# Optimization experiments

Measured on AMD Instinct MI355X. Metric: run time of the kernel, lower is better.

Reference implementation:

```python
import jax, jax.numpy as jnp
import numpy as np

B, C, IMG = 32, 3, 224
NP = 14            # patches per side
PS = IMG // NP     # 16
IN_DIM = C * PS * PS  # 768
D = 768
NH = 12
DH = D // NH       # 64
L = 12
MLP = 4 * D        # 3072
OUT = 1000
S = NP * NP + 1    # 197
EPS = 1e-5


def _pos_embedding(seq_len, dim):
    i = jnp.arange(seq_len, dtype=jnp.float32)[:, None]
    j = jnp.arange(dim, dtype=jnp.float32)[None, :]
    je = j - jnp.mod(j, 2.0)  # even: j, odd: j-1
    angle = i / jnp.power(10000.0, je / dim)
    return jnp.where(jnp.mod(j, 2.0) == 0, jnp.sin(angle), jnp.cos(angle))


def setup_inputs() -> dict:
    key = jax.random.key(0)
    ks = jax.random.split(key, 24)
    s = 0.02
    inp = {
        "x": jax.random.normal(ks[0], (B, C, IMG, IMG), jnp.float32),
        "cls_emb": jax.random.normal(ks[1], (1, 1, D), jnp.float32),
        "pos": _pos_embedding(S, D),
        "Wmap": jax.random.normal(ks[2], (IN_DIM, D), jnp.float32) * s,
        "bmap": jnp.zeros((D,), jnp.float32),
        "ln1_g": jnp.ones((L, D), jnp.float32),
        "ln1_b": jnp.zeros((L, D), jnp.float32),
        "Wq": jax.random.normal(ks[3], (L, NH, DH, DH), jnp.float32) * s,
        "bq": jnp.zeros((L, NH, DH), jnp.float32),
        "Wk": jax.random.normal(ks[4], (L, NH, DH, DH), jnp.float32) * s,
        "bk": jnp.zeros((L, NH, DH), jnp.float32),
        "Wv": jax.random.normal(ks[5], (L, NH, DH, DH), jnp.float32) * s,
        "bv": jnp.zeros((L, NH, DH), jnp.float32),
        "ln2_g": jnp.ones((L, D), jnp.float32),
        "ln2_b": jnp.zeros((L, D), jnp.float32),
        "W1": jax.random.normal(ks[6], (L, D, MLP), jnp.float32) * s,
        "b1": jnp.zeros((L, MLP), jnp.float32),
        "W2": jax.random.normal(ks[7], (L, MLP, D), jnp.float32) * s,
        "b2": jnp.zeros((L, D), jnp.float32),
        "Wc": jax.random.normal(ks[8], (D, OUT), jnp.float32) * s,
        "bc": jnp.zeros((OUT,), jnp.float32),
    }
    return inp


def _layernorm(x, g, b):
    mu = jnp.mean(x, axis=-1, keepdims=True)
    var = jnp.var(x, axis=-1, keepdims=True)
    return (x - mu) * jax.lax.rsqrt(var + EPS) * g + b


def _patchify(x):
    # [B,C,H,W] -> [B, NP*NP, C*PS*PS], flatten order (c, h, w) per patch
    n = x.shape[0]
    x = x.reshape(n, C, NP, PS, NP, PS)
    x = jnp.transpose(x, (0, 2, 4, 1, 3, 5))  # [B, ph, pw, C, PS, PS]
    return x.reshape(n, NP * NP, IN_DIM)


def reference(x, cls_emb, pos, Wmap, bmap, ln1_g, ln1_b, Wq, bq, Wk, bk, Wv, bv,
              ln2_g, ln2_b, W1, b1, W2, b2, Wc, bc):
    patches = _patchify(x)
    tokens = patches @ Wmap + bmap  # [B, NP*NP, D]
    tokens = jnp.concatenate([jnp.broadcast_to(cls_emb, (x.shape[0], 1, D)), tokens], axis=1)
    out = tokens + pos  # [B, S, D]
    scale = 1.0 / jnp.sqrt(jnp.float32(DH))
    for l in range(L):
        xn = _layernorm(out, ln1_g[l], ln1_b[l])
        xh = xn.reshape(xn.shape[0], S, NH, DH)
        q = jnp.einsum('bshd,hed->bshe', xh, Wq[l]) + bq[l]
        k = jnp.einsum('bshd,hed->bshe', xh, Wk[l]) + bk[l]
        v = jnp.einsum('bshd,hed->bshe', xh, Wv[l]) + bv[l]
        att = jax.nn.softmax(jnp.einsum('bqhd,bkhd->bhqk', q, k) * scale, axis=-1)
        attn_out = jnp.einsum('bhqk,bkhd->bqhd', att, v).reshape(out.shape)
        out = out + attn_out
        xn2 = _layernorm(out, ln2_g[l], ln2_b[l])
        h = jax.nn.gelu(xn2 @ W1[l] + b1[l], approximate=False)
        out = out + (h @ W2[l] + b2[l])
    cls = out[:, 0]
    return jax.nn.softmax(cls @ Wc + bc, axis=-1)
```

## Files before the change

kernel.cpp:

```cpp
#include <hip/hip_runtime.h>
#include <hip/hip_bf16.h>
#include <math.h>

#define VB   32
#define VD   768
#define VNH  12
#define VDH  64
#define VL   12
#define VMLP 3072
#define VOUT 1000
#define VS   197
#define VNPAT 196

typedef _Float16 half8 __attribute__((ext_vector_type(8)));
typedef _Float16 half4 __attribute__((ext_vector_type(4)));
typedef float f32x4 __attribute__((ext_vector_type(4)));

static __device__ __forceinline__ unsigned short f2h(float f) {
  _Float16 h = (_Float16)f;
  return __builtin_bit_cast(unsigned short, h);
}
static __device__ __forceinline__ float h2f(unsigned short u) {
  return (float)__builtin_bit_cast(_Float16, u);
}

static __device__ __forceinline__ void gload_lds16(const void* g, void* l) {
  __builtin_amdgcn_global_load_lds(
      (const __attribute__((address_space(1))) unsigned int*)g,
      (__attribute__((address_space(3))) unsigned int*)l, 16, 0, 0);
}

__global__ __launch_bounds__(256) void patchify_kernel(
    const float* __restrict__ x, unsigned short* __restrict__ P) {
  int bp = blockIdx.x;
  int b = bp / VNPAT, p = bp - b * VNPAT;
  int py = p / 14, px = p - py * 14;
  int t = threadIdx.x;
  int iy = t >> 4, ix = t & 15;
#pragma unroll
  for (int c = 0; c < 3; c++) {
    float val = x[(((size_t)(b * 3 + c) * 224) + (py * 16 + iy)) * 224 + px * 16 + ix];
    P[(size_t)bp * 768 + c * 256 + t] = f2h(val);
  }
}

__global__ __launch_bounds__(256) void transpose_kernel(
    const float* __restrict__ W, unsigned short* __restrict__ WT,
    int K, int N) {
  __shared__ float ts[64][65];
  int n0 = blockIdx.x * 64, k0 = blockIdx.y * 64;
  const float* Wl = W + (size_t)blockIdx.z * K * N;
  unsigned short* WTl = WT + (size_t)blockIdx.z * K * N;
  int t = threadIdx.x;
  int r = t >> 4, c4 = (t & 15) * 4;
#pragma unroll
  for (int p = 0; p < 4; ++p) {
    int row = p * 16 + r;
    float4 v = *(const float4*)(Wl + (size_t)(k0 + row) * N + n0 + c4);
    ts[row][c4 + 0] = v.x; ts[row][c4 + 1] = v.y;
    ts[row][c4 + 2] = v.z; ts[row][c4 + 3] = v.w;
  }
  __syncthreads();
#pragma unroll
  for (int p = 0; p < 4; ++p) {
    int n = p * 16 + r;
    ushort4 o;
    o.x = f2h(ts[c4 + 0][n]);
    o.y = f2h(ts[c4 + 1][n]);
    o.z = f2h(ts[c4 + 2][n]);
    o.w = f2h(ts[c4 + 3][n]);
    *(ushort4*)(WTl + (size_t)(n0 + n) * K + k0 + c4) = o;
  }
}

__global__ __launch_bounds__(256) void pack_qkv_kernel(
    const float* __restrict__ Wq, const float* __restrict__ Wk,
    const float* __restrict__ Wv, unsigned short* __restrict__ Wp) {
  size_t idx = (size_t)blockIdx.x * 256 + threadIdx.x;
  int d = idx & 63;
  size_t r = idx >> 6;
  int n = (int)(r % 192);
  size_t lh = r / 192;
  int which = n >> 6, e = n & 63;
  const float* W = which == 0 ? Wq : which == 1 ? Wk : Wv;
  Wp[idx] = f2h(W[(lh * 64 + e) * 64 + d]);
}

__global__ __launch_bounds__(256) void addpos_kernel(
    const float* __restrict__ cls, const float* __restrict__ pos,
    float* __restrict__ out) {
  int bs = blockIdx.x;
  int s = bs % VS;
  int t = threadIdx.x;
  size_t o = (size_t)bs * VD;
#pragma unroll
  for (int j = 0; j < 3; j++) {
    int d = j * 256 + t;
    if (s == 0) out[o + d] = cls[d] + pos[d];
    else        out[o + d] += pos[(size_t)s * VD + d];
  }
}

__global__ __launch_bounds__(256) void ln_kernel(
    const float* __restrict__ x, unsigned short* __restrict__ y,
    const float* __restrict__ g, const float* __restrict__ b) {
  int row = blockIdx.x;
  int t = threadIdx.x;
  const float* xr = x + (size_t)row * VD;
  float v0 = xr[t], v1 = xr[t + 256], v2 = xr[t + 512];
  float s = v0 + v1 + v2;
  float ss = v0 * v0 + v1 * v1 + v2 * v2;
#pragma unroll
  for (int off = 32; off; off >>= 1) {
    s  += __shfl_down(s, off);
    ss += __shfl_down(ss, off);
  }
  __shared__ float red[10];
  int wid = t >> 6, lane = t & 63;
  if (lane == 0) { red[wid] = s; red[4 + wid] = ss; }
  __syncthreads();
  if (t == 0) {
    float S  = red[0] + red[1] + red[2] + red[3];
    float SS = red[4] + red[5] + red[6] + red[7];
    float mu = S * (1.0f / VD);
    float var = SS * (1.0f / VD) - mu * mu;
    red[8] = mu;
    red[9] = rsqrtf(var + 1e-5f);
  }
  __syncthreads();
  float mu = red[8], rs = red[9];
  unsigned short* yr = y + (size_t)row * VD;
  yr[t]       = f2h((v0 - mu) * rs * g[t]       + b[t]);
  yr[t + 256] = f2h((v1 - mu) * rs * g[t + 256] + b[t + 256]);
  yr[t + 512] = f2h((v2 - mu) * rs * g[t + 512] + b[t + 512]);
}

__global__ __launch_bounds__(256) void qkv_gemm(
    const unsigned short* __restrict__ xn,
    const unsigned short* __restrict__ Wp,
    const float* __restrict__ bq, const float* __restrict__ bk,
    const float* __restrict__ bv,
    unsigned short* __restrict__ qh, unsigned short* __restrict__ kh,
    unsigned short* __restrict__ vt) {
  __shared__ unsigned short As[128 * 72];
  __shared__ unsigned short Bs[192 * 72];
  int h = blockIdx.y;
  int bm = blockIdx.x * 128;
  int t = threadIdx.x;
  int srow = t >> 3;
  int scol = (t & 7) * 8;
#pragma unroll
  for (int p = 0; p < 4; ++p) {
    int row = p * 32 + srow;
    int grow = bm + row;
    uint4 val = make_uint4(0u, 0u, 0u, 0u);
    if (grow < VB * VS)
      val = *(const uint4*)(xn + (size_t)grow * VD + h * 64 + scol);
    *(uint4*)(&As[row * 72 + scol]) = val;
  }
#pragma unroll
  for (int p = 0; p < 6; ++p) {
    int row = p * 32 + srow;
    uint4 val = *(const uint4*)(Wp + ((size_t)h * 192 + row) * 64 + scol);
    *(uint4*)(&Bs[row * 72 + scol]) = val;
  }
  __syncthreads();
  int lane = t & 63, wv = t >> 6;
  int wm = (wv & 1) * 64, wn = (wv >> 1) * 96;
  int l15 = lane & 15, l4 = lane >> 4;
  f32x4 acc[4][6] = {};
#pragma unroll
  for (int kk = 0; kk < 64; kk += 32) {
    half8 af[4], bf[6];
#pragma unroll
    for (int i = 0; i < 4; ++i)
      af[i] = *(const half8*)(&As[(wm + i * 16 + l15) * 72 + kk + l4 * 8]);
#pragma unroll
    for (int j = 0; j < 6; ++j)
      bf[j] = *(const half8*)(&Bs[(wn + j * 16 + l15) * 72 + kk + l4 * 8]);
#pragma unroll
    for (int i = 0; i < 4; ++i)
#pragma unroll
      for (int j = 0; j < 6; ++j)
        acc[i][j] = __builtin_amdgcn_mfma_f32_16x16x32_f16(
            af[i], bf[j], acc[i][j], 0, 0, 0);
  }
#pragma unroll
  for (int j = 0; j < 6; ++j) {
    int n = wn + j * 16 + l15;
    int which = n >> 6, e = n & 63;
    const float* bias = which == 0 ? bq : which == 1 ? bk : bv;
    float bval = bias[h * 64 + e];
#pragma unroll
    for (int i = 0; i < 4; ++i) {
#pragma unroll
      for (int r = 0; r < 4; ++r) {
        int tok = bm + wm + i * 16 + l4 * 4 + r;
        if (tok < VB * VS) {
          int b = tok / VS, s = tok - b * VS;
          size_t bh = (size_t)b * VNH + h;
          unsigned short val = f2h(acc[i][j][r] + bval);
          if (which == 0)      qh[(bh * VS + s) * 64 + e] = val;
          else if (which == 1) kh[(bh * VS + s) * 64 + e] = val;
          else                 vt[(bh * 64 + e) * 208 + s] = val;
        }
      }
    }
  }
}

__global__ __launch_bounds__(256) void vt_ztail(unsigned short* __restrict__ vt) {
  int i = blockIdx.x * 256 + threadIdx.x;
  int c = i % 11;
  int rd = i / 11;
  vt[(size_t)rd * 208 + 197 + c] = 0;
}

#define PSTR 212
__global__ __launch_bounds__(256) void attn_mfma(
    const unsigned short* __restrict__ qh,
    const unsigned short* __restrict__ kh,
    const unsigned short* __restrict__ vt,
    float* __restrict__ out) {
  int bh = blockIdx.x;
  int qt = blockIdx.y;
  int t = threadIdx.x;
  int w = t >> 6, lane = t & 63;
  int l15 = lane & 15, l4 = lane >> 4;
  __shared__ unsigned short Pl[4][16 * PSTR];

  int qrow = qt * 64 + w * 16 + l15;
  const unsigned short* qbase = qh + ((size_t)bh * VS) * 64;
  const unsigned short* kbase = kh + ((size_t)bh * VS) * 64;
  half8 qf0 = *(const half8*)(qbase + (size_t)qrow * 64 + l4 * 8);
  half8 qf1 = *(const half8*)(qbase + (size_t)qrow * 64 + 32 + l4 * 8);

  f32x4 S[13];
#pragma unroll
  for (int j = 0; j < 13; ++j) {
    half8 b0 = *(const half8*)(kbase + (size_t)(j * 16 + l15) * 64 + l4 * 8);
    half8 b1 = *(const half8*)(kbase + (size_t)(j * 16 + l15) * 64 + 32 + l4 * 8);
    f32x4 c = {};
    c = __builtin_amdgcn_mfma_f32_16x16x32_f16(qf0, b0, c, 0, 0, 0);
    c = __builtin_amdgcn_mfma_f32_16x16x32_f16(qf1, b1, c, 0, 0, 0);
    S[j] = c;
  }
  float m4[4] = {-3.0e38f, -3.0e38f, -3.0e38f, -3.0e38f};
#pragma unroll
  for (int j = 0; j < 13; ++j) {
#pragma unroll
    for (int r = 0; r < 4; ++r) {
      float s = S[j][r] * 0.125f;
      if (j == 12 && l15 > 4) s = -3.0e38f;
      S[j][r] = s;
      m4[r] = fmaxf(m4[r], s);
    }
  }
#pragma unroll
  for (int off = 1; off < 16; off <<= 1) {
#pragma unroll
    for (int r = 0; r < 4; ++r) m4[r] = fmaxf(m4[r], __shfl_xor(m4[r], off));
  }
  float ls[4] = {0.f, 0.f, 0.f, 0.f};
#pragma unroll
  for (int j = 0; j < 13; ++j) {
#pragma unroll
    for (int r = 0; r < 4; ++r) {
      float p = __expf(S[j][r] - m4[r]);
      S[j][r] = p;
      ls[r] += p;
    }
  }
#pragma unroll
  for (int off = 1; off < 16; off <<= 1) {
#pragma unroll
    for (int r = 0; r < 4; ++r) ls[r] += __shfl_xor(ls[r], off);
  }
  unsigned short* Pw = &Pl[w][0];
#pragma unroll
  for (int j = 0; j < 13; ++j) {
#pragma unroll
    for (int r = 0; r < 4; ++r)
      Pw[(l4 * 4 + r) * PSTR + j * 16 + l15] = f2h(S[j][r]);
  }
  const unsigned short* vbase = vt + (size_t)bh * 64 * 208;
  f32x4 O[4] = {};
#pragma unroll
  for (int jk = 0; jk < 13; ++jk) {
    half4 a = *(const half4*)(Pw + l15 * PSTR + jk * 16 + l4 * 4);
#pragma unroll
    for (int jn = 0; jn < 4; ++jn) {
      half4 b = *(const half4*)(vbase + (size_t)(jn * 16 + l15) * 208 + jk * 16 + l4 * 4);
      O[jn] = __builtin_amdgcn_mfma_f32_16x16x16f16(a, b, O[jn], 0, 0, 0);
    }
  }
  int b = bh / VNH, h = bh - (bh / VNH) * VNH;
  float linv[4];
#pragma unroll
  for (int r = 0; r < 4; ++r) linv[r] = 1.0f / ls[r];
#pragma unroll
  for (int r = 0; r < 4; ++r) {
    int qr = qt * 64 + w * 16 + l4 * 4 + r;
    if (qr < VS) {
      float* op = out + ((size_t)b * VS + qr) * VD + h * VDH;
#pragma unroll
      for (int jn = 0; jn < 4; ++jn)
        op[jn * 16 + l15] += O[jn][r] * linv[r];
    }
  }
}

template <int EPI, int REMAP>
__global__ __launch_bounds__(256) void gemm_h(
    const unsigned short* __restrict__ A,
    const unsigned short* __restrict__ Bt,
    const float* __restrict__ bias, float* __restrict__ C,
    int M, int N, int K, int KS) {
  __shared__ unsigned short As[128 * 64];
  __shared__ unsigned short Bs[128 * 64];
  int t = threadIdx.x;
  int bm = blockIdx.y * 128, bn = blockIdx.x * 128;
  int lane = t & 63, w = t >> 6;
  int wm = (w & 1) * 64, wn = (w >> 1) * 64;
  int l15 = lane & 15, l4 = lane >> 4;
  int lrow = lane >> 3, lcol = (lane & 7) * 8;
  f32x4 acc[4][4] = {};
  int kbeg = blockIdx.z * KS;
  if (EPI == 3) C += (size_t)blockIdx.z * M * N;
  for (int k0 = kbeg; k0 < kbeg + KS; k0 += 64) {
#pragma unroll
    for (int p = 0; p < 4; ++p) {
      int r0 = w * 32 + p * 8;
      int ga = bm + r0;
      if (ga > M - 8) ga = M - 8;
      gload_lds16(A + (size_t)(ga + lrow) * K + k0 + lcol, &As[r0 * 64]);
      gload_lds16(Bt + (size_t)(bn + r0 + lrow) * K + k0 + lcol, &Bs[r0 * 64]);
    }
    __syncthreads();
#pragma unroll
    for (int kk = 0; kk < 64; kk += 32) {
      half8 af[4], bf[4];
#pragma unroll
      for (int i = 0; i < 4; ++i)
        af[i] = *(const half8*)(&As[(wm + i * 16 + l15) * 64 + kk + l4 * 8]);
#pragma unroll
      for (int j = 0; j < 4; ++j)
        bf[j] = *(const half8*)(&Bs[(wn + j * 16 + l15) * 64 + kk + l4 * 8]);
#pragma unroll
      for (int i = 0; i < 4; ++i)
#pragma unroll
        for (int j = 0; j < 4; ++j)
          acc[i][j] = __builtin_amdgcn_mfma_f32_16x16x32_f16(
              af[i], bf[j], acc[i][j], 0, 0, 0);
    }
    __syncthreads();
  }
#pragma unroll
  for (int i = 0; i < 4; ++i) {
#pragma unroll
    for (int j = 0; j < 4; ++j) {
#pragma unroll
      for (int r = 0; r < 4; ++r) {
        int row = bm + wm + i * 16 + l4 * 4 + r;
        int col = bn + wn + j * 16 + l15;
        if (row < M) {
          if (EPI == 3) {
            C[(size_t)row * N + col] = acc[i][j][r];
          } else {
            float val = acc[i][j][r] + bias[col];
            if (EPI == 0) {
              int crow = REMAP ? (row + row / 196 + 1) : row;
              C[(size_t)crow * N + col] = val;
            } else if (EPI == 1) {
              val = 0.5f * val * (1.0f + erff(val * 0.70710678118654752440f));
              ((unsigned short*)C)[(size_t)row * N + col] = f2h(val);
            } else {
              C[(size_t)row * N + col] += val;
            }
          }
        }
      }
    }
  }
}

__global__ __launch_bounds__(256) void mlp2_reduce(
    const float* __restrict__ p0, const float* __restrict__ p1,
    const float* __restrict__ bias, float* __restrict__ out) {
  size_t idx = ((size_t)blockIdx.x * 256 + threadIdx.x) * 4;
  int col = (int)(idx % VD);
  float4 a = *(const float4*)(p0 + idx);
  float4 b = *(const float4*)(p1 + idx);
  float4 bi = *(const float4*)(bias + col);
  float4 o = *(const float4*)(out + idx);
  o.x += a.x + b.x + bi.x;
  o.y += a.y + b.y + bi.y;
  o.z += a.z + b.z + bi.z;
  o.w += a.w + b.w + bi.w;
  *(float4*)(out + idx) = o;
}

__global__ __launch_bounds__(256) void cls_logits(
    const float* __restrict__ out_act, const float* __restrict__ Wc,
    const float* __restrict__ bc, float* __restrict__ lbuf) {
  int b = blockIdx.y;
  int n0 = blockIdx.x * 250;
  int t = threadIdx.x;
  __shared__ float xs[768];
  const float* xr = out_act + (size_t)b * VS * VD;
  xs[t] = xr[t]; xs[t + 256] = xr[t + 256]; xs[t + 512] = xr[t + 512];
  __syncthreads();
  if (t < 250) {
    int col = n0 + t;
    float acc = bc[col];
#pragma unroll 4
    for (int d = 0; d < VD; ++d) acc += xs[d] * Wc[(size_t)d * VOUT + col];
    lbuf[(size_t)b * VOUT + col] = acc;
  }
}

__global__ __launch_bounds__(256) void cls_softmax(
    const float* __restrict__ lbuf, float* __restrict__ y) {
  int b = blockIdx.x;
  int t = threadIdx.x;
  __shared__ float logit[VOUT];
  __shared__ float red[10];
  for (int j = t; j < VOUT; j += 256) logit[j] = lbuf[(size_t)b * VOUT + j];
  __syncthreads();
  float m = -1e30f;
  for (int j = t; j < VOUT; j += 256) m = fmaxf(m, logit[j]);
#pragma unroll
  for (int off = 32; off; off >>= 1) m = fmaxf(m, __shfl_down(m, off));
  if ((t & 63) == 0) red[t >> 6] = m;
  __syncthreads();
  if (t == 0) red[8] = fmaxf(fmaxf(red[0], red[1]), fmaxf(red[2], red[3]));
  __syncthreads();
  float M = red[8];
  float s = 0.f;
  for (int j = t; j < VOUT; j += 256) {
    float e = expf(logit[j] - M);
    logit[j] = e;
    s += e;
  }
#pragma unroll
  for (int off = 32; off; off >>= 1) s += __shfl_down(s, off);
  if ((t & 63) == 0) red[4 + (t >> 6)] = s;
  __syncthreads();
  if (t == 0) red[9] = red[4] + red[5] + red[6] + red[7];
  __syncthreads();
  float inv = 1.0f / red[9];
  for (int j = t; j < VOUT; j += 256) y[(size_t)b * VOUT + j] = logit[j] * inv;
}

extern "C" void kernel_launch(void* const* d_in, const int* in_sizes, int n_in,
                              void* d_out, int out_size, void* d_ws, size_t ws_size,
                              hipStream_t stream) {
  const float* x      = (const float*)d_in[0];
  const float* cls    = (const float*)d_in[1];
  const float* pos    = (const float*)d_in[2];
  const float* Wmap   = (const float*)d_in[3];
  const float* bmap   = (const float*)d_in[4];
  const float* ln1_g  = (const float*)d_in[5];
  const float* ln1_b  = (const float*)d_in[6];
  const float* Wq     = (const float*)d_in[7];
  const float* bq     = (const float*)d_in[8];
  const float* Wk     = (const float*)d_in[9];
  const float* bk     = (const float*)d_in[10];
  const float* Wv     = (const float*)d_in[11];
  const float* bv     = (const float*)d_in[12];
  const float* ln2_g  = (const float*)d_in[13];
  const float* ln2_b  = (const float*)d_in[14];
  const float* W1     = (const float*)d_in[15];
  const float* b1     = (const float*)d_in[16];
  const float* W2     = (const float*)d_in[17];
  const float* b2     = (const float*)d_in[18];
  const float* Wc     = (const float*)d_in[19];
  const float* bc     = (const float*)d_in[20];
  float* yout = (float*)d_out;

  const size_t nBS  = (size_t)VB * VS;
  const size_t nBSD = nBS * VD;
  const size_t nQK  = (size_t)VB * VNH * VS * 64;
  char* base = (char*)d_ws;
  size_t off = 0;
  float* out_act = (float*)(base + off);      off += nBSD * 4;
  unsigned short* xnb = (unsigned short*)(base + off); off += nBSD * 2;
  unsigned short* qhb = (unsigned short*)(base + off); off += nQK * 2 + 65536;
  unsigned short* khb = (unsigned short*)(base + off); off += nQK * 2 + 65536;
  unsigned short* vtb = (unsigned short*)(base + off); off += (size_t)VB * VNH * 64 * 208 * 2;
  unsigned short* hbuf = (unsigned short*)(base + off); off += nBS * VMLP * 2;
  unsigned short* wmapT = (unsigned short*)(base + off); off += (size_t)VD * VD * 2;
  unsigned short* w1T = (unsigned short*)(base + off);   off += (size_t)VL * VMLP * VD * 2;
  unsigned short* w2T = (unsigned short*)(base + off);   off += (size_t)VL * VD * VMLP * 2;
  unsigned short* wqkv = (unsigned short*)(base + off);  off += (size_t)VL * VNH * 192 * 64 * 2;
  float* part = (float*)xnb;
  float* lbuf = (float*)qhb;

  transpose_kernel<<<dim3(12, 12, 1), 256, 0, stream>>>(Wmap, wmapT, VD, VD);
  transpose_kernel<<<dim3(48, 12, VL), 256, 0, stream>>>(W1, w1T, VD, VMLP);
  transpose_kernel<<<dim3(12, 48, VL), 256, 0, stream>>>(W2, w2T, VMLP, VD);
  pack_qkv_kernel<<<(VL * VNH * 192 * 64) / 256, 256, 0, stream>>>(Wq, Wk, Wv, wqkv);

  patchify_kernel<<<VB * VNPAT, 256, 0, stream>>>(x, hbuf);
  gemm_h<0, 1><<<dim3(6, 49), 256, 0, stream>>>(
      hbuf, wmapT, bmap, out_act, VB * VNPAT, VD, VD, VD);
  addpos_kernel<<<(int)nBS, 256, 0, stream>>>(cls, pos, out_act);

  for (int l = 0; l < VL; l++) {
    ln_kernel<<<(int)nBS, 256, 0, stream>>>(out_act, xnb,
                                            ln1_g + (size_t)l * VD,
                                            ln1_b + (size_t)l * VD);
    qkv_gemm<<<dim3(50, VNH), 256, 0, stream>>>(
        xnb, wqkv + (size_t)l * VNH * 192 * 64,
        bq + (size_t)l * VNH * VDH, bk + (size_t)l * VNH * VDH,
        bv + (size_t)l * VNH * VDH, qhb, khb, vtb);
    vt_ztail<<<(VB * VNH * 64 * 11) / 256, 256, 0, stream>>>(vtb);
    attn_mfma<<<dim3(VB * VNH, 4), 256, 0, stream>>>(qhb, khb, vtb, out_act);
    ln_kernel<<<(int)nBS, 256, 0, stream>>>(out_act, xnb,
                                            ln2_g + (size_t)l * VD,
                                            ln2_b + (size_t)l * VD);
    gemm_h<1, 0><<<dim3(24, 50), 256, 0, stream>>>(
        xnb, w1T + (size_t)l * VMLP * VD, b1 + (size_t)l * VMLP,
        (float*)hbuf, (int)nBS, VMLP, VD, VD);
    gemm_h<3, 0><<<dim3(6, 50, 2), 256, 0, stream>>>(
        hbuf, w2T + (size_t)l * VD * VMLP, nullptr,
        part, (int)nBS, VD, VMLP, VMLP / 2);
    mlp2_reduce<<<(int)(nBSD / 1024), 256, 0, stream>>>(
        part, part + nBSD, b2 + (size_t)l * VD, out_act);
  }
  cls_logits<<<dim3(4, VB), 256, 0, stream>>>(out_act, Wc, bc, lbuf);
  cls_softmax<<<VB, 256, 0, stream>>>(lbuf, yout);
}
```

Before: 4.074 ms.

## Add 256x256-tile double-buffered MFMA GEMM for MLP layers

Adds a new 512-thread GEMM kernel with 256x256 output tiles, direct global-to-LDS loads into a double-buffered 128KB LDS region, and an interleaved schedule of LDS reads, staging, and MFMA phases with explicit waitcnt, sched barriers and setprio. It replaces the previous GEMM for both MLP up-projection (with GELU epilogue) and split-K down-projection. The larger tiles raise arithmetic intensity and the manual pipelining is meant to overlap memory traffic with MFMA work. The trade-off is fewer blocks (300 and 150) on a 256-CU device, which risks poor occupancy and tail imbalance, plus fragile hand-tuned synchronization.

```diff
diff --git a/kernel.cpp b/kernel.cpp
--- a/kernel.cpp
+++ b/kernel.cpp
@@ -382,6 +382,163 @@
       }
     }
   }
+}
+
+#define GSB0() __builtin_amdgcn_sched_barrier(0)
+
+template <int EPI>
+__global__ __launch_bounds__(512, 2) void gemm256(
+    const unsigned short* __restrict__ A,
+    const unsigned short* __restrict__ Bt,
+    const float* __restrict__ bias, float* __restrict__ C,
+    int M, int N, int K, int KS) {
+  __shared__ uint4 lds4[8192];
+  char* ldsb = (char*)lds4;
+  int t = threadIdx.x;
+  int w = t >> 6, lane = t & 63;
+  int wm = w >> 2, wn = w & 3;
+  int l15 = lane & 15, l4 = lane >> 4;
+  int bm = blockIdx.y * 256, bn = blockIdx.x * 256;
+  int kbeg = blockIdx.z * KS;
+  int kmax = kbeg + KS - 64;
+  if (EPI == 3) C += (size_t)blockIdx.z * M * N;
+  int laneoff = ((l15 << 6) | (l4 << 4)) ^ ((l15 & 8) << 2);
+  int cl = lane ^ ((lane & 32) >> 4);
+  int rin = cl >> 2, c8 = (cl & 3) << 3;
+
+  f32x4 acc[8][4] = {};
+  half8 af[4][2], bf0[2][2], bf1[2][2];
+
+#define STAGE_A(sl, half, kt)                                                  \
+  {                                                                            \
+    int kc = (kt); if (kc > kmax) kc = kmax;                                   \
+    _Pragma("unroll") for (int q = 0; q < 2; ++q) {                            \
+      int s = (half) * 16 + q * 8 + w;                                         \
+      int grow = bm + (s >> 1) * 16 + rin;                                     \
+      if (grow >= M) grow = M - 1;                                             \
+      gload_lds16(A + (size_t)grow * K + kc + ((s & 1) << 5) + c8,             \
+                  ldsb + (sl) * 65536 + s * 1024);                             \
+    }                                                                          \
+  }
+#define STAGE_B(sl, half, kt)                                                  \
+  {                                                                            \
+    int kc = (kt); if (kc > kmax) kc = kmax;                                   \
+    _Pragma("unroll") for (int q = 0; q < 2; ++q) {                            \
+      int s = (half) * 16 + q * 8 + w;                                         \
+      gload_lds16(Bt + (size_t)(bn + (s >> 1) * 16 + rin) * K + kc +           \
+                      ((s & 1) << 5) + c8,                                     \
+                  ldsb + (sl) * 65536 + 32768 + s * 1024);                     \
+    }                                                                          \
+  }
+#define PH_LOADA(sl, mq)                                                       \
+  {                                                                            \
+    _Pragma("unroll") for (int mf = 0; mf < 4; ++mf) {                         \
+      int sub = (wm * 8 + (mq) * 4 + mf) * 2048;                               \
+      af[mf][0] = *(const half8*)(ldsb + (sl) * 65536 + sub + laneoff);        \
+      af[mf][1] = *(const half8*)(ldsb + (sl) * 65536 + sub + 1024 + laneoff); \
+    }                                                                          \
+  }
+#define PH_LOADB(sl, nq, BF)                                                   \
+  {                                                                            \
+    _Pragma("unroll") for (int nf = 0; nf < 2; ++nf) {                         \
+      int sub = (wn * 4 + (nq) * 2 + nf) * 2048;                               \
+      BF[nf][0] = *(const half8*)(ldsb + (sl) * 65536 + 32768 + sub + laneoff);\
+      BF[nf][1] = *(const half8*)(ldsb + (sl) * 65536 + 32768 + sub + 1024 + laneoff); \
+    }                                                                          \
+  }
+#define PH_MMA(mq, nq, BF)                                                     \
+  __builtin_amdgcn_s_setprio(1);                                               \
+  _Pragma("unroll") for (int mf = 0; mf < 4; ++mf)                             \
+  _Pragma("unroll") for (int nf = 0; nf < 2; ++nf) {                           \
+    acc[(mq)*4+mf][(nq)*2+nf] = __builtin_amdgcn_mfma_f32_16x16x32_f16(        \
+        af[mf][0], BF[nf][0], acc[(mq)*4+mf][(nq)*2+nf], 0, 0, 0);             \
+    acc[(mq)*4+mf][(nq)*2+nf] = __builtin_amdgcn_mfma_f32_16x16x32_f16(        \
+        af[mf][1], BF[nf][1], acc[(mq)*4+mf][(nq)*2+nf], 0, 0, 0);             \
+  }                                                                            \
+  __builtin_amdgcn_s_setprio(0);
+#define GBAR() __builtin_amdgcn_s_barrier()
+#define WAIT_LGKM0() { asm volatile("s_waitcnt lgkmcnt(0)" ::: "memory"); GSB0(); }
+#define WAIT_VM4()   { asm volatile("s_waitcnt vmcnt(4)"   ::: "memory"); GSB0(); }
+
+  STAGE_A(0, 0, kbeg); STAGE_A(0, 1, kbeg);
+  STAGE_B(0, 0, kbeg); STAGE_B(0, 1, kbeg);
+  STAGE_B(1, 0, kbeg + 64); STAGE_B(1, 1, kbeg + 64);
+  WAIT_VM4();
+  GBAR(); GSB0();
+
+  int NITER = KS >> 7;
+  for (int j = 0; j < NITER; ++j) {
+    int k0 = kbeg + j * 128;
+    PH_LOADA(0, 0); PH_LOADB(0, 0, bf0);
+    STAGE_A(1, 0, k0 + 64);
+    GBAR(); WAIT_LGKM0();
+    PH_MMA(0, 0, bf0);
+    GBAR(); GSB0();
+    PH_LOADB(0, 1, bf1);
+    STAGE_A(1, 1, k0 + 64);
+    GBAR(); WAIT_LGKM0();
+    PH_MMA(0, 1, bf1);
+    GBAR(); GSB0();
+    PH_LOADA(0, 1);
+    STAGE_B(0, 0, k0 + 128);
+    GBAR(); WAIT_LGKM0();
+    PH_MMA(1, 0, bf0);
+    GBAR(); GSB0();
+    STAGE_B(0, 1, k0 + 128);
+    GBAR(); WAIT_LGKM0();
+    PH_MMA(1, 1, bf1);
+    WAIT_VM4();
+    GBAR(); GSB0();
+    PH_LOADA(1, 0); PH_LOADB(1, 0, bf0);
+    STAGE_A(0, 0, k0 + 128);
+    GBAR(); WAIT_LGKM0();
+    PH_MMA(0, 0, bf0);
+    GBAR(); GSB0();
+    PH_LOADB(1, 1, bf1);
+    STAGE_A(0, 1, k0 + 128);
+    GBAR(); WAIT_LGKM0();
+    PH_MMA(0, 1, bf1);
+    GBAR(); GSB0();
+    PH_LOADA(1, 1);
+    STAGE_B(1, 0, k0 + 192);
+    GBAR(); WAIT_LGKM0();
+    PH_MMA(1, 0, bf0);
+    GBAR(); GSB0();
+    STAGE_B(1, 1, k0 + 192);
+    GBAR(); WAIT_LGKM0();
+    PH_MMA(1, 1, bf1);
+    WAIT_VM4();
+    GBAR(); GSB0();
+  }
+
+#pragma unroll
+  for (int m = 0; m < 8; ++m) {
+#pragma unroll
+    for (int n = 0; n < 4; ++n) {
+      int col = bn + wn * 64 + n * 16 + l15;
+#pragma unroll
+      for (int r = 0; r < 4; ++r) {
+        int row = bm + wm * 128 + m * 16 + l4 * 4 + r;
+        if (row < M) {
+          if (EPI == 1) {
+            float val = acc[m][n][r] + bias[col];
+            val = 0.5f * val * (1.0f + erff(val * 0.70710678118654752440f));
+            ((unsigned short*)C)[(size_t)row * N + col] = f2h(val);
+          } else {
+            C[(size_t)row * N + col] = acc[m][n][r];
+          }
+        }
+      }
+    }
+  }
+#undef STAGE_A
+#undef STAGE_B
+#undef PH_LOADA
+#undef PH_LOADB
+#undef PH_MMA
+#undef GBAR
+#undef WAIT_LGKM0
+#undef WAIT_VM4
 }
 
 __global__ __launch_bounds__(256) void mlp2_reduce(
@@ -519,10 +676,10 @@
     ln_kernel<<<(int)nBS, 256, 0, stream>>>(out_act, xnb,
                                             ln2_g + (size_t)l * VD,
                                             ln2_b + (size_t)l * VD);
-    gemm_h<1, 0><<<dim3(24, 50), 256, 0, stream>>>(
+    gemm256<1><<<dim3(VMLP / 256, 25, 1), 512, 0, stream>>>(
         xnb, w1T + (size_t)l * VMLP * VD, b1 + (size_t)l * VMLP,
         (float*)hbuf, (int)nBS, VMLP, VD, VD);
-    gemm_h<3, 0><<<dim3(6, 50, 2), 256, 0, stream>>>(
+    gemm256<3><<<dim3(VD / 256, 25, 2), 512, 0, stream>>>(
         hbuf, w2T + (size_t)l * VD * VMLP, nullptr,
         part, (int)nBS, VD, VMLP, VMLP / 2);
     mlp2_reduce<<<(int)(nBSD / 1024), 256, 0, stream>>>(
```

Result: faster. 3.743 ms (-8.1%).

## Add 256x256-tile double-buffered MFMA GEMM for the MLP layers

Applied to the files above, without the earlier changes.

Introduces a new 512-thread GEMM kernel with 256x256 output tiles. It stages A and B from global memory directly into LDS, double-buffered, and interleaves the LDS fragment loads with MFMA issue under explicit barriers, waitcnts and setprio. Both MLP GEMMs (W1 with the GELU epilogue, and the split-K W2) switch from the older 128-class gemm_h to this kernel to get more data reuse per tile and better overlap of loads with compute. The larger tiles give fewer blocks: the W1 grid is 12x25 and the W2 grid is 3x25x2, which risks poor occupancy and wave quantization on the W2 GEMM. The hand-scheduled sync is also fragile.

```diff
diff --git a/kernel.cpp b/kernel.cpp
--- a/kernel.cpp
+++ b/kernel.cpp
@@ -382,6 +382,144 @@
       }
     }
   }
+}
+
+#define GSB0() __builtin_amdgcn_sched_barrier(0)
+
+template <int EPI>
+__global__ __launch_bounds__(512, 2) void gemm256(
+    const unsigned short* __restrict__ A,
+    const unsigned short* __restrict__ Bt,
+    const float* __restrict__ bias, float* __restrict__ C,
+    int M, int N, int K, int KS) {
+  __shared__ uint4 lds4[8192];
+  char* ldsb = (char*)lds4;
+  int t = threadIdx.x;
+  int w = t >> 6, lane = t & 63;
+  int wm = w >> 2, wn = w & 3;
+  int l15 = lane & 15, l4 = lane >> 4;
+  int bm = blockIdx.y * 256, bn = blockIdx.x * 256;
+  int kbeg = blockIdx.z * KS;
+  int kmax = kbeg + KS - 64;
+  if (EPI == 3) C += (size_t)blockIdx.z * M * N;
+  int laneoff = ((l15 << 6) | (l4 << 4)) ^ ((l15 & 8) << 2);
+  int cl = lane ^ ((lane & 32) >> 4);
+  int rin = cl >> 2, c8 = (cl & 3) << 3;
+
+  size_t aOff[4], bOff[4];
+  int ldsOffA[4], ldsOffB[4];
+#pragma unroll
+  for (int j = 0; j < 4; ++j) {
+    int s = w + 8 * j;
+    int ar = bm + (s >> 1) * 16 + rin; if (ar >= M) ar = M - 1;
+    aOff[j] = (size_t)ar * K + ((s & 1) << 5) + c8;
+    int br = bn + (s >> 1) * 16 + rin;
+    bOff[j] = (size_t)br * K + ((s & 1) << 5) + c8;
+    ldsOffA[j] = s * 1024;
+    ldsOffB[j] = 32768 + s * 1024;
+  }
+  int rdA = wm * 8 * 2048 + laneoff;
+  int rdB = 32768 + wn * 4 * 2048 + laneoff;
+
+  f32x4 acc[8][4] = {};
+  half8 af[4][2], bf[4][2];
+
+#define STAGE_A(sl, kk)                                                        \
+  { _Pragma("unroll") for (int j = 0; j < 4; ++j)                              \
+      gload_lds16(A + aOff[j] + (kk), ldsb + (sl) * 65536 + ldsOffA[j]); }
+#define STAGE_B(sl, kk)                                                        \
+  { _Pragma("unroll") for (int j = 0; j < 4; ++j)                              \
+      gload_lds16(Bt + bOff[j] + (kk), ldsb + (sl) * 65536 + ldsOffB[j]); }
+#define LOAD_AF(sl, mq)                                                        \
+  { _Pragma("unroll") for (int mf = 0; mf < 4; ++mf) {                         \
+      af[mf][0] = *(const half8*)(ldsb + (sl) * 65536 + rdA + (mq) * 8192 +    \
+                                  mf * 2048);                                  \
+      af[mf][1] = *(const half8*)(ldsb + (sl) * 65536 + rdA + (mq) * 8192 +    \
+                                  mf * 2048 + 1024); } }
+#define LOAD_BF(sl)                                                            \
+  { _Pragma("unroll") for (int nf = 0; nf < 4; ++nf) {                         \
+      bf[nf][0] = *(const half8*)(ldsb + (sl) * 65536 + rdB + nf * 2048);      \
+      bf[nf][1] = *(const half8*)(ldsb + (sl) * 65536 + rdB + nf * 2048 +      \
+                                  1024); } }
+#define MMA32(mq)                                                              \
+  __builtin_amdgcn_s_setprio(1);                                               \
+  _Pragma("unroll") for (int mf = 0; mf < 4; ++mf)                             \
+  _Pragma("unroll") for (int nf = 0; nf < 4; ++nf) {                           \
+    acc[(mq)*4+mf][nf] = __builtin_amdgcn_mfma_f32_16x16x32_f16(               \
+        af[mf][0], bf[nf][0], acc[(mq)*4+mf][nf], 0, 0, 0);                    \
+    acc[(mq)*4+mf][nf] = __builtin_amdgcn_mfma_f32_16x16x32_f16(               \
+        af[mf][1], bf[nf][1], acc[(mq)*4+mf][nf], 0, 0, 0);                    \
+  }                                                                            \
+  __builtin_amdgcn_s_setprio(0);
+#define GBAR() __builtin_amdgcn_s_barrier()
+#define WAIT_LGKM0() { asm volatile("s_waitcnt lgkmcnt(0)" ::: "memory"); GSB0(); }
+#define WAIT_VM4()   { asm volatile("s_waitcnt vmcnt(4)"   ::: "memory"); GSB0(); }
+
+  STAGE_A(0, kbeg);
+  STAGE_B(0, kbeg);
+  STAGE_B(1, kbeg + 64);
+  int kA = kbeg, kB = kbeg + 64;
+  WAIT_VM4();
+  GBAR(); GSB0();
+
+  int NITER = KS >> 7;
+  for (int j = 0; j < NITER; ++j) {
+    LOAD_AF(0, 0); LOAD_BF(0);
+    kA += 64; if (kA > kmax) kA = kmax;
+    STAGE_A(1, kA);
+    GBAR(); WAIT_LGKM0();
+    MMA32(0);
+    GBAR(); GSB0();
+    LOAD_AF(0, 1);
+    kB += 64; if (kB > kmax) kB = kmax;
+    STAGE_B(0, kB);
+    GBAR(); WAIT_LGKM0();
+    MMA32(1);
+    WAIT_VM4();
+    GBAR(); GSB0();
+    LOAD_AF(1, 0); LOAD_BF(1);
+    kA += 64; if (kA > kmax) kA = kmax;
+    STAGE_A(0, kA);
+    GBAR(); WAIT_LGKM0();
+    MMA32(0);
+    GBAR(); GSB0();
+    LOAD_AF(1, 1);
+    kB += 64; if (kB > kmax) kB = kmax;
+    STAGE_B(1, kB);
+    GBAR(); WAIT_LGKM0();
+    MMA32(1);
+    WAIT_VM4();
+    GBAR(); GSB0();
+  }
+
+#pragma unroll
+  for (int m = 0; m < 8; ++m) {
+#pragma unroll
+    for (int n = 0; n < 4; ++n) {
+      int col = bn + wn * 64 + n * 16 + l15;
+#pragma unroll
+      for (int r = 0; r < 4; ++r) {
+        int row = bm + wm * 128 + m * 16 + l4 * 4 + r;
+        if (row < M) {
+          if (EPI == 1) {
+            float val = acc[m][n][r] + bias[col];
+            val = 0.5f * val * (1.0f + erff(val * 0.70710678118654752440f));
+            ((unsigned short*)C)[(size_t)row * N + col] = f2h(val);
+          } else {
+            C[(size_t)row * N + col] = acc[m][n][r];
+          }
+        }
+      }
+    }
+  }
+#undef STAGE_A
+#undef STAGE_B
+#undef LOAD_AF
+#undef LOAD_BF
+#undef MMA32
+#undef GBAR
+#undef WAIT_LGKM0
+#undef WAIT_VM4
 }
 
 __global__ __launch_bounds__(256) void mlp2_reduce(
@@ -519,10 +657,10 @@
     ln_kernel<<<(int)nBS, 256, 0, stream>>>(out_act, xnb,
                                             ln2_g + (size_t)l * VD,
                                             ln2_b + (size_t)l * VD);
-    gemm_h<1, 0><<<dim3(24, 50), 256, 0, stream>>>(
+    gemm256<1><<<dim3(VMLP / 256, 25, 1), 512, 0, stream>>>(
         xnb, w1T + (size_t)l * VMLP * VD, b1 + (size_t)l * VMLP,
         (float*)hbuf, (int)nBS, VMLP, VD, VD);
-    gemm_h<3, 0><<<dim3(6, 50, 2), 256, 0, stream>>>(
+    gemm256<3><<<dim3(VD / 256, 25, 2), 512, 0, stream>>>(
         hbuf, w2T + (size_t)l * VD * VMLP, nullptr,
         part, (int)nBS, VD, VMLP, VMLP / 2);
     mlp2_reduce<<<(int)(nBSD / 1024), 256, 0, stream>>>(
```

After: 3.753 ms. -7.9%, faster.
